# Kernel tuning notes

Measured on AMD Instinct MI355X. Metric: run time of the kernel, lower is better.

## Reference

```python
import jax, jax.numpy as jnp
import numpy as np

P, M_DIM, R_DIM = 1024, 64, 32


def setup_inputs() -> dict:
    key = jax.random.key(0)
    k1, k2, k3, k4, k5 = jax.random.split(key, 5)
    hidden_state = jax.random.normal(k1, (P, M_DIM), dtype=jnp.float32)
    corr_index = jax.random.normal(k2, (P, P, 2), dtype=jnp.float32)
    nei_index = jax.random.randint(k3, (P, P), 0, 2, dtype=jnp.int32)
    # params: rela_embed Linear(2, r_dim); attention Linear(2*m_dim + r_dim, 1)
    # init_weights_attr: normal(mean=0, std=0.2), bias 0
    W_rela = 0.2 * jax.random.normal(k4, (2, R_DIM), dtype=jnp.float32)
    b_rela = jnp.zeros((R_DIM,), dtype=jnp.float32)
    W_att = 0.2 * jax.random.normal(k5, (2 * M_DIM + R_DIM, 1), dtype=jnp.float32)
    b_att = jnp.zeros((1,), dtype=jnp.float32)
    return {
        "hidden_state": hidden_state,
        "corr_index": corr_index,
        "nei_index": nei_index,
        "W_rela": W_rela,
        "b_rela": b_rela,
        "W_att": W_att,
        "b_att": b_att,
    }


def reference(hidden_state, corr_index, nei_index, W_rela, b_rela, W_att, b_att):
    m = hidden_state.shape[1]
    r = W_rela.shape[1]
    mask = nei_index > 0  # [P, P]; entry (i, j): j is a neighbor of i

    # rela_embed -> relu (dropout is identity at eval time)
    rela = jax.nn.relu(jnp.einsum('ijc,cr->ijr', corr_index, W_rela) + b_rela)  # [P,P,r]

    # attention Linear over cat([rela, h_i, h_j]); decompose the weight so we
    # never materialize the [P,P, r+2m] concatenation.
    w = W_att[:, 0]
    w_r, w_hi, w_nei = w[:r], w[r:r + m], w[r + m:]
    scores = (jnp.einsum('ijr,r->ij', rela, w_r)
              + (hidden_state @ w_hi)[:, None]
              + (hidden_state @ w_nei)[None, :]
              + b_att[0])  # [P,P]

    # masked-out entries get 0, then every exact zero becomes -1e-6 (as in source)
    Pos = jnp.where(mask, scores, 0.0)
    Pos = jnp.where(Pos == 0.0, -1e-6, Pos)
    Pos = jax.nn.softmax(Pos, axis=1)

    # weighted scatter-sum: H[i,j] = mask * Pos[i,j] * h_j ; sum over j
    social_tensor = jnp.einsum('ij,jm->im', Pos * mask.astype(Pos.dtype), hidden_state)
    return social_tensor
```

## Files before the change

kernel.cpp:

```cpp
#include <hip/hip_runtime.h>

#define PP   1024
#define MM   64
#define RR   32
#define ROWS 4
#define TPB  1024
#define NW   (TPB / 64)

__global__ __launch_bounds__(256) void proj_kernel(
    const float* __restrict__ hidden,
    const float* __restrict__ W_att,
    const float* __restrict__ b_att,
    float* __restrict__ ws)
{
    const int wid  = threadIdx.x >> 6;
    const int lane = threadIdx.x & 63;
    const int p = blockIdx.x * 4 + wid;

    float h = hidden[p * MM + lane];
    float a = h * W_att[RR + lane];
    float b = h * W_att[RR + MM + lane];
#pragma unroll
    for (int off = 32; off > 0; off >>= 1) {
        a += __shfl_down(a, off, 64);
        b += __shfl_down(b, off, 64);
    }
    if (lane == 0) {
        ws[p]      = a + b_att[0];
        ws[PP + p] = b;
    }
}

__global__ __launch_bounds__(TPB, 4) void social_kernel(
    const float* __restrict__ hidden,
    const float* __restrict__ corr,
    const int*   __restrict__ nei,
    const float* __restrict__ W_rela,
    const float* __restrict__ b_rela,
    const float* __restrict__ W_att,
    const float* __restrict__ ws,
    float* __restrict__ out)
{
    __shared__ float4 q4[PP];
    __shared__ float4 red[NW];
    __shared__ float  partf[NW][ROWS][MM];

    const int t    = threadIdx.x;
    const int lane = t & 63;
    const int wid  = t >> 6;
    const int i0   = blockIdx.x * ROWS;

    float4 W0[RR / 4], W1[RR / 4], Bv[RR / 4], Wr[RR / 4];
    {
        const float4* W_rela4 = (const float4*)W_rela;
        const float4* b4      = (const float4*)b_rela;
        const float4* wa4     = (const float4*)W_att;
#pragma unroll
        for (int k = 0; k < RR / 4; ++k) {
            W0[k] = W_rela4[k];
            W1[k] = W_rela4[RR / 4 + k];
            Bv[k] = b4[k];
            Wr[k] = wa4[k];
        }
    }
    float hib[ROWS];
#pragma unroll
    for (int r = 0; r < ROWS; ++r) hib[r] = ws[i0 + r];

    const int j = t;
    const float hn = ws[PP + j];

    float2 c[ROWS];
    int    nv[ROWS];
#pragma unroll
    for (int r = 0; r < ROWS; ++r) {
        c[r]  = ((const float2*)corr)[(i0 + r) * PP + j];
        nv[r] = nei[(i0 + r) * PP + j];
    }

    float pos[ROWS], msk[ROWS];
#pragma unroll
    for (int r = 0; r < ROWS; ++r) {
        float s = 0.f;
#pragma unroll
        for (int k = 0; k < RR / 4; ++k) {
            float t0 = fmaxf(fmaf(c[r].x, W0[k].x, fmaf(c[r].y, W1[k].x, Bv[k].x)), 0.f);
            float t1 = fmaxf(fmaf(c[r].x, W0[k].y, fmaf(c[r].y, W1[k].y, Bv[k].y)), 0.f);
            float t2 = fmaxf(fmaf(c[r].x, W0[k].z, fmaf(c[r].y, W1[k].z, Bv[k].z)), 0.f);
            float t3 = fmaxf(fmaf(c[r].x, W0[k].w, fmaf(c[r].y, W1[k].w, Bv[k].w)), 0.f);
            s = fmaf(t0, Wr[k].x, s);
            s = fmaf(t1, Wr[k].y, s);
            s = fmaf(t2, Wr[k].z, s);
            s = fmaf(t3, Wr[k].w, s);
        }
        const float score = s + hib[r] + hn;
        float p = (nv[r] > 0) ? score : 0.0f;
        p = (p == 0.0f) ? -1e-6f : p;
        pos[r] = p;
        msk[r] = (nv[r] > 0) ? 1.0f : 0.0f;
    }

    float m4[ROWS];
#pragma unroll
    for (int r = 0; r < ROWS; ++r) m4[r] = pos[r];
#pragma unroll
    for (int off = 32; off > 0; off >>= 1) {
#pragma unroll
        for (int r = 0; r < ROWS; ++r)
            m4[r] = fmaxf(m4[r], __shfl_xor(m4[r], off, 64));
    }
    if (lane == 0) red[wid] = make_float4(m4[0], m4[1], m4[2], m4[3]);
    __syncthreads();
#pragma unroll
    for (int w = 0; w < NW; ++w) {
        const float4 v = red[w];
        m4[0] = fmaxf(m4[0], v.x);
        m4[1] = fmaxf(m4[1], v.y);
        m4[2] = fmaxf(m4[2], v.z);
        m4[3] = fmaxf(m4[3], v.w);
    }

    float e4[ROWS], s4[ROWS];
#pragma unroll
    for (int r = 0; r < ROWS; ++r) {
        e4[r] = __expf(pos[r] - m4[r]);
        s4[r] = e4[r];
    }
#pragma unroll
    for (int off = 32; off > 0; off >>= 1) {
#pragma unroll
        for (int r = 0; r < ROWS; ++r)
            s4[r] += __shfl_xor(s4[r], off, 64);
    }
    __syncthreads();
    if (lane == 0) red[wid] = make_float4(s4[0], s4[1], s4[2], s4[3]);
    __syncthreads();
    {
        float a0 = 0.f, a1 = 0.f, a2 = 0.f, a3 = 0.f;
#pragma unroll
        for (int w = 0; w < NW; ++w) {
            const float4 v = red[w];
            a0 += v.x; a1 += v.y; a2 += v.z; a3 += v.w;
        }
        s4[0] = a0; s4[1] = a1; s4[2] = a2; s4[3] = a3;
    }

    q4[j] = make_float4(e4[0] * msk[0] / s4[0],
                        e4[1] * msk[1] / s4[1],
                        e4[2] * msk[2] / s4[2],
                        e4[3] * msk[3] / s4[3]);
    __syncthreads();

    const int q_idx = lane >> 4;
    const int mslot = lane & 15;
    float4 acc[ROWS];
#pragma unroll
    for (int r = 0; r < ROWS; ++r) acc[r] = make_float4(0.f, 0.f, 0.f, 0.f);

#pragma unroll 4
    for (int it = 0; it < 16; ++it) {
        const int jj = wid * 4 + q_idx + it * 64;
        const float4 h4 = ((const float4*)hidden)[jj * (MM / 4) + mslot];
        const float4 q  = q4[jj];
        acc[0].x = fmaf(q.x, h4.x, acc[0].x);
        acc[0].y = fmaf(q.x, h4.y, acc[0].y);
        acc[0].z = fmaf(q.x, h4.z, acc[0].z);
        acc[0].w = fmaf(q.x, h4.w, acc[0].w);
        acc[1].x = fmaf(q.y, h4.x, acc[1].x);
        acc[1].y = fmaf(q.y, h4.y, acc[1].y);
        acc[1].z = fmaf(q.y, h4.z, acc[1].z);
        acc[1].w = fmaf(q.y, h4.w, acc[1].w);
        acc[2].x = fmaf(q.z, h4.x, acc[2].x);
        acc[2].y = fmaf(q.z, h4.y, acc[2].y);
        acc[2].z = fmaf(q.z, h4.z, acc[2].z);
        acc[2].w = fmaf(q.z, h4.w, acc[2].w);
        acc[3].x = fmaf(q.w, h4.x, acc[3].x);
        acc[3].y = fmaf(q.w, h4.y, acc[3].y);
        acc[3].z = fmaf(q.w, h4.z, acc[3].z);
        acc[3].w = fmaf(q.w, h4.w, acc[3].w);
    }

#pragma unroll
    for (int off = 16; off <= 32; off <<= 1) {
#pragma unroll
        for (int r = 0; r < ROWS; ++r) {
            acc[r].x += __shfl_xor(acc[r].x, off, 64);
            acc[r].y += __shfl_xor(acc[r].y, off, 64);
            acc[r].z += __shfl_xor(acc[r].z, off, 64);
            acc[r].w += __shfl_xor(acc[r].w, off, 64);
        }
    }
    if (lane < 16) {
#pragma unroll
        for (int r = 0; r < ROWS; ++r)
            ((float4*)&partf[wid][r][0])[mslot] = acc[r];
    }
    __syncthreads();

    if (t < ROWS * MM) {
        const int row = t >> 6;
        const int col = t & 63;
        float s = 0.f;
#pragma unroll
        for (int w = 0; w < NW; ++w) s += partf[w][row][col];
        out[(i0 + row) * MM + col] = s;
    }
}

extern "C" void kernel_launch(void* const* d_in, const int* in_sizes, int n_in,
                              void* d_out, int out_size, void* d_ws, size_t ws_size,
                              hipStream_t stream)
{
    const float* hidden = (const float*)d_in[0];
    const float* corr   = (const float*)d_in[1];
    const int*   nei    = (const int*)d_in[2];
    const float* W_rela = (const float*)d_in[3];
    const float* b_rela = (const float*)d_in[4];
    const float* W_att  = (const float*)d_in[5];
    const float* b_att  = (const float*)d_in[6];
    float* ws  = (float*)d_ws;
    float* out = (float*)d_out;

    proj_kernel<<<PP / 4, 256, 0, stream>>>(hidden, W_att, b_att, ws);
    social_kernel<<<PP / ROWS, TPB, 0, stream>>>(hidden, corr, nei, W_rela,
                                                 b_rela, W_att, ws, out);
}
```

Baseline: 86.87 us.

## Fuse projection kernel into social kernel and drop softmax max reduction

Removes the separate projection launch: each block now recomputes the neighbor projection for every column j and the self projection for its own rows directly from hidden_state. It also computes the softmax as exp(p)/sum without subtracting the row maximum, which removes one block-wide reduction and a barrier. In exchange, every block re-reads the whole hidden matrix with strided per-thread loads. The softmax without the max shift can overflow for large scores, so its safety depends on the score magnitudes.

After: 90.21 us. 1.04x slower.

```diff
diff --git a/kernel.cpp b/kernel.cpp
--- a/kernel.cpp
+++ b/kernel.cpp
@@ -7,48 +7,65 @@
 #define TPB  1024
 #define NW   (TPB / 64)
 
-__global__ __launch_bounds__(256) void proj_kernel(
-    const float* __restrict__ hidden,
-    const float* __restrict__ W_att,
-    const float* __restrict__ b_att,
-    float* __restrict__ ws)
-{
-    const int wid  = threadIdx.x >> 6;
-    const int lane = threadIdx.x & 63;
-    const int p = blockIdx.x * 4 + wid;
-
-    float h = hidden[p * MM + lane];
-    float a = h * W_att[RR + lane];
-    float b = h * W_att[RR + MM + lane];
-#pragma unroll
-    for (int off = 32; off > 0; off >>= 1) {
-        a += __shfl_down(a, off, 64);
-        b += __shfl_down(b, off, 64);
-    }
-    if (lane == 0) {
-        ws[p]      = a + b_att[0];
-        ws[PP + p] = b;
-    }
-}
-
-__global__ __launch_bounds__(TPB, 4) void social_kernel(
+__global__ __launch_bounds__(TPB) void social_fused(
     const float* __restrict__ hidden,
     const float* __restrict__ corr,
     const int*   __restrict__ nei,
     const float* __restrict__ W_rela,
     const float* __restrict__ b_rela,
     const float* __restrict__ W_att,
-    const float* __restrict__ ws,
+    const float* __restrict__ b_att,
     float* __restrict__ out)
 {
     __shared__ float4 q4[PP];
     __shared__ float4 red[NW];
+    __shared__ float  his[ROWS];
     __shared__ float  partf[NW][ROWS][MM];
 
     const int t    = threadIdx.x;
     const int lane = t & 63;
     const int wid  = t >> 6;
     const int i0   = blockIdx.x * ROWS;
+
+    float2 c[ROWS];
+    int    nv[ROWS];
+#pragma unroll
+    for (int r = 0; r < ROWS; ++r) {
+        c[r]  = ((const float2*)corr)[(i0 + r) * PP + t];
+        nv[r] = nei[(i0 + r) * PP + t];
+    }
+
+    float hn = 0.f;
+    {
+        const float4* h4 = (const float4*)(hidden + t * MM);
+        const float4* wn = (const float4*)(W_att + RR + MM);
+#pragma unroll
+        for (int k = 0; k < MM / 4; ++k) {
+            const float4 h = h4[k];
+            const float4 w = wn[k];
+            hn = fmaf(h.x, w.x, hn);
+            hn = fmaf(h.y, w.y, hn);
+            hn = fmaf(h.z, w.z, hn);
+            hn = fmaf(h.w, w.w, hn);
+        }
+    }
+
+    if (t >= i0 && t < i0 + ROWS) {
+        const float4* h4 = (const float4*)(hidden + t * MM);
+        const float4* wh = (const float4*)(W_att + RR);
+        float hi = 0.f;
+#pragma unroll
+        for (int k = 0; k < MM / 4; ++k) {
+            const float4 h = h4[k];
+            const float4 w = wh[k];
+            hi = fmaf(h.x, w.x, hi);
+            hi = fmaf(h.y, w.y, hi);
+            hi = fmaf(h.z, w.z, hi);
+            hi = fmaf(h.w, w.w, hi);
+        }
+        his[t - i0] = hi + b_att[0];
+    }
+    __syncthreads();
 
     float4 W0[RR / 4], W1[RR / 4], Bv[RR / 4], Wr[RR / 4];
     {
@@ -63,22 +80,8 @@
             Wr[k] = wa4[k];
         }
     }
-    float hib[ROWS];
-#pragma unroll
-    for (int r = 0; r < ROWS; ++r) hib[r] = ws[i0 + r];
-
-    const int j = t;
-    const float hn = ws[PP + j];
-
-    float2 c[ROWS];
-    int    nv[ROWS];
-#pragma unroll
-    for (int r = 0; r < ROWS; ++r) {
-        c[r]  = ((const float2*)corr)[(i0 + r) * PP + j];
-        nv[r] = nei[(i0 + r) * PP + j];
-    }
-
-    float pos[ROWS], msk[ROWS];
+
+    float e4[ROWS], msk[ROWS], s4[ROWS];
 #pragma unroll
     for (int r = 0; r < ROWS; ++r) {
         float s = 0.f;
@@ -93,46 +96,20 @@
             s = fmaf(t2, Wr[k].z, s);
             s = fmaf(t3, Wr[k].w, s);
         }
-        const float score = s + hib[r] + hn;
+        const float score = s + his[r] + hn;
         float p = (nv[r] > 0) ? score : 0.0f;
         p = (p == 0.0f) ? -1e-6f : p;
-        pos[r] = p;
+        e4[r]  = __expf(p);
         msk[r] = (nv[r] > 0) ? 1.0f : 0.0f;
-    }
-
-    float m4[ROWS];
-#pragma unroll
-    for (int r = 0; r < ROWS; ++r) m4[r] = pos[r];
-#pragma unroll
-    for (int off = 32; off > 0; off >>= 1) {
-#pragma unroll
-        for (int r = 0; r < ROWS; ++r)
-            m4[r] = fmaxf(m4[r], __shfl_xor(m4[r], off, 64));
-    }
-    if (lane == 0) red[wid] = make_float4(m4[0], m4[1], m4[2], m4[3]);
-    __syncthreads();
-#pragma unroll
-    for (int w = 0; w < NW; ++w) {
-        const float4 v = red[w];
-        m4[0] = fmaxf(m4[0], v.x);
-        m4[1] = fmaxf(m4[1], v.y);
-        m4[2] = fmaxf(m4[2], v.z);
-        m4[3] = fmaxf(m4[3], v.w);
-    }
-
-    float e4[ROWS], s4[ROWS];
-#pragma unroll
-    for (int r = 0; r < ROWS; ++r) {
-        e4[r] = __expf(pos[r] - m4[r]);
-        s4[r] = e4[r];
-    }
+        s4[r]  = e4[r];
+    }
+
 #pragma unroll
     for (int off = 32; off > 0; off >>= 1) {
 #pragma unroll
         for (int r = 0; r < ROWS; ++r)
             s4[r] += __shfl_xor(s4[r], off, 64);
     }
-    __syncthreads();
     if (lane == 0) red[wid] = make_float4(s4[0], s4[1], s4[2], s4[3]);
     __syncthreads();
     {
@@ -145,7 +122,7 @@
         s4[0] = a0; s4[1] = a1; s4[2] = a2; s4[3] = a3;
     }
 
-    q4[j] = make_float4(e4[0] * msk[0] / s4[0],
+    q4[t] = make_float4(e4[0] * msk[0] / s4[0],
                         e4[1] * msk[1] / s4[1],
                         e4[2] * msk[2] / s4[2],
                         e4[3] * msk[3] / s4[3]);
@@ -218,10 +195,8 @@
     const float* b_rela = (const float*)d_in[4];
     const float* W_att  = (const float*)d_in[5];
     const float* b_att  = (const float*)d_in[6];
-    float* ws  = (float*)d_ws;
     float* out = (float*)d_out;
 
-    proj_kernel<<<PP / 4, 256, 0, stream>>>(hidden, W_att, b_att, ws);
-    social_kernel<<<PP / ROWS, TPB, 0, stream>>>(hidden, corr, nei, W_rela,
-                                                 b_rela, W_att, ws, out);
+    social_fused<<<PP / ROWS, TPB, 0, stream>>>(hidden, corr, nei, W_rela,
+                                                b_rela, W_att, b_att, out);
 }
```
